# Kernel optimization log

Measured on AMD Instinct MI355X. Metric: run time of the kernel, lower is better.

## Reference

```python
import jax, jax.numpy as jnp
import numpy as np

B, N, E, ED, H, HID, OUT = 128, 100, 3200, 8, 4, 16, 32


def _ln(x, g, b):
    m = x.mean(-1, keepdims=True)
    v = ((x - m) ** 2).mean(-1, keepdims=True)
    return (x - m) / jnp.sqrt(v + 1e-5) * g + b


def _seg_softmax(logits, seg, n):
    # logits: [Etot, H], seg: [Etot] target node ids
    m = jax.ops.segment_max(logits, seg, num_segments=n)
    ex = jnp.exp(logits - m[seg])
    s = jax.ops.segment_sum(ex, seg, num_segments=n)
    return ex / (s[seg] + 1e-16)


def _tconv(x, src, dst, ea, Wq, bq, Wk, bk, Wv, bv, We, Ws, bs, heads, ch, n):
    # PyG TransformerConv, concat=False, root_weight=True, beta=False
    q = (x @ Wq.T + bq).reshape(-1, heads, ch)
    k = (x @ Wk.T + bk).reshape(-1, heads, ch)
    v = (x @ Wv.T + bv).reshape(-1, heads, ch)
    e = (ea @ We.T).reshape(-1, heads, ch)
    alpha = (q[dst] * (k[src] + e)).sum(-1) / jnp.sqrt(jnp.float32(ch))  # [Etot,H]
    alpha = _seg_softmax(alpha, dst, n)
    msg = (v[src] + e) * alpha[..., None]
    out = jax.ops.segment_sum(msg, dst, num_segments=n)  # [n,H,ch]
    out = out.mean(axis=1)  # concat=False -> head mean
    return out + x @ Ws.T + bs


def setup_inputs() -> dict:
    key = jax.random.key(0)
    ks = jax.random.split(key, 32)
    d = {}
    d['nodes_feats'] = jax.random.randint(ks[0], (B, N, 1), 0, 5).astype(jnp.float32)
    d['edge_index'] = jax.random.randint(ks[1], (B, 2, E), 0, N).astype(jnp.int32)
    d['edge_attr'] = jax.random.normal(ks[2], (B, E, ED), jnp.float32)
    d['agent_id'] = jax.random.randint(ks[3], (B, 1), 0, N).astype(jnp.int32)
    s = 0.1
    d['entity_embed'] = jax.random.normal(ks[4], (5, 4), jnp.float32)
    d['W1'] = jax.random.normal(ks[5], (HID, 4 + ED), jnp.float32) * s
    d['b1'] = jnp.zeros((HID,), jnp.float32)
    d['W2'] = jax.random.normal(ks[6], (HID, HID), jnp.float32) * s
    d['b2'] = jnp.zeros((HID,), jnp.float32)
    d['W3'] = jax.random.normal(ks[7], (HID, HID), jnp.float32) * s
    d['b3'] = jnp.zeros((HID,), jnp.float32)
    d['ln_g'] = jnp.ones((HID,), jnp.float32)
    d['ln_b'] = jnp.zeros((HID,), jnp.float32)
    i = 8
    for pre, ch, outd in (('g1', HID, HID), ('g2', OUT, OUT)):
        d[pre + '_Wq'] = jax.random.normal(ks[i + 0], (H * ch, HID), jnp.float32) * s
        d[pre + '_bq'] = jnp.zeros((H * ch,), jnp.float32)
        d[pre + '_Wk'] = jax.random.normal(ks[i + 1], (H * ch, HID), jnp.float32) * s
        d[pre + '_bk'] = jnp.zeros((H * ch,), jnp.float32)
        d[pre + '_Wv'] = jax.random.normal(ks[i + 2], (H * ch, HID), jnp.float32) * s
        d[pre + '_bv'] = jnp.zeros((H * ch,), jnp.float32)
        d[pre + '_We'] = jax.random.normal(ks[i + 3], (H * ch, ED), jnp.float32) * s
        d[pre + '_Ws'] = jax.random.normal(ks[i + 4], (outd, HID), jnp.float32) * s
        d[pre + '_bs'] = jnp.zeros((outd,), jnp.float32)
        i += 5
    return d


def reference(nodes_feats, edge_index, edge_attr, agent_id, entity_embed,
              W1, b1, W2, b2, W3, b3, ln_g, ln_b,
              g1_Wq, g1_bq, g1_Wk, g1_bk, g1_Wv, g1_bv, g1_We, g1_Ws, g1_bs,
              g2_Wq, g2_bq, g2_Wk, g2_bk, g2_Wv, g2_bv, g2_We, g2_Ws, g2_bs):
    n_tot = B * N
    # batched graph -> flat graph with per-batch node offsets
    offs = (jnp.arange(B, dtype=edge_index.dtype) * N)[:, None, None]
    ei = (edge_index + offs).transpose(1, 0, 2).reshape(2, -1)  # [2, B*E]
    src, dst = ei[0], ei[1]
    x = nodes_feats.reshape(-1, 1)            # [n_tot, 1]
    ea = edge_attr.reshape(-1, ED)            # [B*E, ED]

    # Embedding message-passing layer (aggr='add')
    etype = x[:, 0].astype(jnp.int32)[src]
    emb = entity_embed[etype]                  # [Etot, 4]
    h = jnp.concatenate([emb, ea], axis=1)
    h = _ln(jax.nn.relu(h @ W1.T + b1), ln_g, ln_b)
    h = _ln(jax.nn.relu(h @ W2.T + b2), ln_g, ln_b)
    h = _ln(jax.nn.relu(h @ W3.T + b3), ln_g, ln_b)
    z = jax.ops.segment_sum(h, dst, num_segments=n_tot)  # [n_tot, 16]

    a = _tconv(z, src, dst, ea, g1_Wq, g1_bq, g1_Wk, g1_bk, g1_Wv, g1_bv,
               g1_We, g1_Ws, g1_bs, H, HID, n_tot)
    a = _tconv(a, src, dst, ea, g2_Wq, g2_bq, g2_Wk, g2_bk, g2_Wv, g2_bv,
               g2_We, g2_Ws, g2_bs, H, OUT, n_tot)
    a = jax.nn.relu(a).reshape(B, N, OUT)
    # graph_aggr == 'agent': gather the agent node per batch
    out = jnp.take_along_axis(a, agent_id[:, :, None].astype(jnp.int32), axis=1)
    return out[:, 0, :]  # [B, OUT]
```

## Files before the change

kernel.cpp:

```cpp
#include <hip/hip_runtime.h>
#include <math.h>
#include <stdint.h>

#define Bb   128
#define Nn   100
#define Ee   3200
#define NTOT (Bb*Nn)
#define ETOT (Bb*Ee)



__global__ __launch_bounds__(256) void k_csr(const int* __restrict__ ei,
                                             const int* __restrict__ agent,
                                             int* __restrict__ off,
                                             int2* __restrict__ cpair,
                                             int* __restrict__ mark)
{
    int b = ((blockIdx.x & 7) << 4) + (blockIdx.x >> 3);
    int t = threadIdx.x;
    __shared__ int cnt[128];
    __shared__ int exc[128];
    __shared__ int cur[128];
    if (t < 128) cnt[t] = 0;
    if (t < Nn) mark[b * Nn + t] = 0;
    __syncthreads();
    const int* eis = ei + (size_t)b * 2 * Ee;
    const int* eid = eis + Ee;
    for (int e = t; e < Ee; e += 256) atomicAdd(&cnt[eid[e]], 1);
    __syncthreads();
    if (t < 128) exc[t] = cnt[t];
    __syncthreads();
    for (int d = 1; d < 128; d <<= 1) {
        int v = 0;
        if (t < 128 && t >= d) v = exc[t - d];
        __syncthreads();
        if (t < 128) exc[t] += v;
        __syncthreads();
    }
    if (t < 128) { int e0 = exc[t] - cnt[t]; exc[t] = e0; cur[t] = e0; }
    __syncthreads();
    if (t < Nn) off[b * Nn + t] = b * Ee + exc[t];
    if (b == Bb - 1 && t == 0) off[NTOT] = ETOT;
    for (int e = t; e < Ee; e += 256) {
        int dst = eid[e];
        int idx = atomicAdd(&cur[dst], 1);
        cpair[b * Ee + idx] = make_int2(eis[e] + b * Nn, b * Ee + e);
    }
    int an = agent[b];
    __syncthreads();
    if (t == 0) mark[b * Nn + an] = 1;
    for (int e = t; e < Ee; e += 256) {
        if (eid[e] == an) mark[b * Nn + eis[e]] = 1;
    }
}


__device__ __forceinline__ void ln_reg(float* h, const float* __restrict__ g,
                                       const float* __restrict__ b) {
    float s = 0.f;
#pragma unroll
    for (int c = 0; c < 16; c++) s += h[c];
    float m = s * 0.0625f;
    float v = 0.f;
#pragma unroll
    for (int c = 0; c < 16; c++) { float d = h[c] - m; v += d * d; }
    float r = rsqrtf(v * 0.0625f + 1e-5f);
#pragma unroll
    for (int c = 0; c < 16; c++) h[c] = (h[c] - m) * r * g[c] + b[c];
}

__global__ __launch_bounds__(256) void k_mlpz(
    const float* __restrict__ nf, const float* __restrict__ ea, const float* __restrict__ ee,
    const float* __restrict__ W1, const float* __restrict__ b1,
    const float* __restrict__ W2, const float* __restrict__ b2,
    const float* __restrict__ W3, const float* __restrict__ b3,
    const float* __restrict__ lg, const float* __restrict__ lb,
    const float* __restrict__ Wq, const float* __restrict__ bq,
    const float* __restrict__ Wk, const float* __restrict__ bk,
    const float* __restrict__ Wv, const float* __restrict__ bv,
    const int* __restrict__ off, const int2* __restrict__ cpair,
    float* __restrict__ z, float* __restrict__ q1, float* __restrict__ k1, float* __restrict__ v1)
{
    __shared__ float hs[4][64][17];
    __shared__ int sdeg[4];
    int lane = threadIdx.x & 63;
    int wid  = threadIdx.x >> 6;
    int n    = (blockIdx.x & 7) * (NTOT / 8) + (blockIdx.x >> 3) * 4 + wid;

    int o0 = off[n];
    int deg = off[n + 1] - o0;
    if (lane == 0) sdeg[wid] = deg;
    __syncthreads();
    int mdeg = max(max(sdeg[0], sdeg[1]), max(sdeg[2], sdeg[3]));
    int chunks = (mdeg + 63) >> 6;

    float zp = 0.f;
    for (int ch = 0; ch < chunks; ch++) {
        int i = ch * 64 + lane;
        float h3[16];
        if (i < deg) {
            int2 p = cpair[o0 + i];
            int et = (int)nf[p.x];
            float in[12];
#pragma unroll
            for (int j = 0; j < 4; j++) in[j] = ee[et * 4 + j];
            const float4* ea4 = (const float4*)(ea + (size_t)p.y * 8);
            float4 ua = ea4[0], ub = ea4[1];
            in[4] = ua.x; in[5] = ua.y; in[6] = ua.z; in[7] = ua.w;
            in[8] = ub.x; in[9] = ub.y; in[10] = ub.z; in[11] = ub.w;

            float h1[16];
#pragma unroll
            for (int c = 0; c < 16; c++) {
                float s = b1[c];
#pragma unroll
                for (int j = 0; j < 12; j++) s = fmaf(W1[c * 12 + j], in[j], s);
                h1[c] = fmaxf(s, 0.f);
            }
            ln_reg(h1, lg, lb);
            float h2[16];
#pragma unroll
            for (int c = 0; c < 16; c++) {
                float s = b2[c];
#pragma unroll
                for (int j = 0; j < 16; j++) s = fmaf(W2[c * 16 + j], h1[j], s);
                h2[c] = fmaxf(s, 0.f);
            }
            ln_reg(h2, lg, lb);
#pragma unroll
            for (int c = 0; c < 16; c++) {
                float s = b3[c];
#pragma unroll
                for (int j = 0; j < 16; j++) s = fmaf(W3[c * 16 + j], h2[j], s);
                h3[c] = fmaxf(s, 0.f);
            }
            ln_reg(h3, lg, lb);
        } else {
#pragma unroll
            for (int c = 0; c < 16; c++) h3[c] = 0.f;
        }
#pragma unroll
        for (int c = 0; c < 16; c++) hs[wid][lane][c] = h3[c];
        __syncthreads();
        int g = lane >> 4, c = lane & 15;
        float s = 0.f;
#pragma unroll
        for (int k = 0; k < 16; k++) s += hs[wid][g * 16 + k][c];
        s += __shfl_xor(s, 16);
        s += __shfl_xor(s, 32);
        zp += s;
        __syncthreads();
    }

    if (lane < 16) z[n * 16 + lane] = zp;

    float aq = bq[lane], ak = bk[lane], av = bv[lane];
#pragma unroll
    for (int j = 0; j < 16; j++) {
        float zj = __shfl(zp, j, 16);
        aq = fmaf(Wq[lane * 16 + j], zj, aq);
        ak = fmaf(Wk[lane * 16 + j], zj, ak);
        av = fmaf(Wv[lane * 16 + j], zj, av);
    }
    q1[n * 64 + lane] = aq;
    k1[n * 64 + lane] = ak;
    v1[n * 64 + lane] = av;
}


__global__ __launch_bounds__(256) void k_attn1(
    const float* __restrict__ ea,
    const float* __restrict__ q1, const float* __restrict__ k1, const float* __restrict__ v1,
    const float* __restrict__ We, const float* __restrict__ Ws, const float* __restrict__ bs,
    const float* __restrict__ z, const int* __restrict__ mark,
    const int* __restrict__ off, const int2* __restrict__ cpair,
    float* __restrict__ a1)
{
    int lane = threadIdx.x & 63;
    int wid  = threadIdx.x >> 6;
    int n    = (blockIdx.x & 7) * (NTOT / 8) + (blockIdx.x >> 3) * 4 + wid;

    if (!mark[n]) return;

    float wer[8];
#pragma unroll
    for (int j = 0; j < 8; j++) wer[j] = We[lane * 8 + j];
    float ql = q1[n * 64 + lane];

    int o0 = off[n];
    int deg = off[n + 1] - o0;

    float m = -1e30f, l = 0.f, acc = 0.f;
    int i = 0;
    for (; i + 2 <= deg; i += 2) {
        int2 pA = cpair[o0 + i];
        int2 pB = cpair[o0 + i + 1];
        const float4* eaA = (const float4*)(ea + (size_t)pA.y * 8);
        const float4* eaB = (const float4*)(ea + (size_t)pB.y * 8);
        float4 a0v = eaA[0], a1v = eaA[1], b0v = eaB[0], b1v = eaB[1];
        float eA = wer[0] * a0v.x + wer[1] * a0v.y + wer[2] * a0v.z + wer[3] * a0v.w
                 + wer[4] * a1v.x + wer[5] * a1v.y + wer[6] * a1v.z + wer[7] * a1v.w;
        float eB = wer[0] * b0v.x + wer[1] * b0v.y + wer[2] * b0v.z + wer[3] * b0v.w
                 + wer[4] * b1v.x + wer[5] * b1v.y + wer[6] * b1v.z + wer[7] * b1v.w;
        float kA = k1[(size_t)pA.x * 64 + lane];
        float kB = k1[(size_t)pB.x * 64 + lane];
        float vA = v1[(size_t)pA.x * 64 + lane];
        float vB = v1[(size_t)pB.x * 64 + lane];
        float tA = ql * (kA + eA);
        float tB = ql * (kB + eB);
        tA += __shfl_xor(tA, 1, 16);  tB += __shfl_xor(tB, 1, 16);
        tA += __shfl_xor(tA, 2, 16);  tB += __shfl_xor(tB, 2, 16);
        tA += __shfl_xor(tA, 4, 16);  tB += __shfl_xor(tB, 4, 16);
        tA += __shfl_xor(tA, 8, 16);  tB += __shfl_xor(tB, 8, 16);
        float lA = tA * 0.25f;
        float lB = tB * 0.25f;
        float nm = fmaxf(m, fmaxf(lA, lB));
        float sc = __expf(m - nm);
        float wA = __expf(lA - nm);
        float wB = __expf(lB - nm);
        acc = acc * sc + wA * (vA + eA) + wB * (vB + eB);
        l   = l * sc + wA + wB;
        m   = nm;
    }
    for (; i < deg; i++) {
        int2 p = cpair[o0 + i];
        const float4* ea4 = (const float4*)(ea + (size_t)p.y * 8);
        float4 u0 = ea4[0], u1 = ea4[1];
        float el = wer[0] * u0.x + wer[1] * u0.y + wer[2] * u0.z + wer[3] * u0.w
                 + wer[4] * u1.x + wer[5] * u1.y + wer[6] * u1.z + wer[7] * u1.w;
        float kl = k1[(size_t)p.x * 64 + lane];
        float t = ql * (kl + el);
        t += __shfl_xor(t, 1, 16);
        t += __shfl_xor(t, 2, 16);
        t += __shfl_xor(t, 4, 16);
        t += __shfl_xor(t, 8, 16);
        float logit = t * 0.25f;
        float nm = fmaxf(m, logit);
        float sc = __expf(m - nm);
        float w  = __expf(logit - nm);
        float vl = v1[(size_t)p.x * 64 + lane];
        acc = acc * sc + w * (vl + el);
        l   = l * sc + w;
        m   = nm;
    }
    float y = (deg > 0) ? (acc / l) : 0.f;
    y += __shfl_xor(y, 16);
    y += __shfl_xor(y, 32);
    y *= 0.25f;

    if (lane < 16) {
        float r = bs[lane];
#pragma unroll
        for (int j = 0; j < 16; j++) r = fmaf(Ws[lane * 16 + j], z[n * 16 + j], r);
        a1[n * 16 + lane] = y + r;
    }
}


__global__ __launch_bounds__(256) void k_g2(
    const float* __restrict__ ea, const float* __restrict__ a1, const int* __restrict__ agent,
    const float* __restrict__ Wq, const float* __restrict__ bq,
    const float* __restrict__ Wk, const float* __restrict__ bk,
    const float* __restrict__ Wv, const float* __restrict__ bv,
    const float* __restrict__ We, const float* __restrict__ Ws, const float* __restrict__ bs,
    const int* __restrict__ off, const int2* __restrict__ cpair,
    float* __restrict__ out)
{
    __shared__ float sm[4][64], sl[4][64], sa0[4][64], sa1[4][64];
    int b = ((blockIdx.x & 7) << 4) + (blockIdx.x >> 3);
    int lane = threadIdx.x & 63;
    int w = threadIdx.x >> 6;
    int n = b * Nn + agent[b];
    int v0 = lane * 2, v1i = lane * 2 + 1;

    float aa[16];
#pragma unroll
    for (int j = 0; j < 16; j++) aa[j] = a1[n * 16 + j];

    float wk0[16], wk1[16], wv0[16], wv1[16], we0[8], we1[8];
#pragma unroll
    for (int j = 0; j < 16; j++) {
        wk0[j] = Wk[v0 * 16 + j];  wk1[j] = Wk[v1i * 16 + j];
        wv0[j] = Wv[v0 * 16 + j];  wv1[j] = Wv[v1i * 16 + j];
    }
#pragma unroll
    for (int j = 0; j < 8; j++) { we0[j] = We[v0 * 8 + j]; we1[j] = We[v1i * 8 + j]; }

    float q0 = bq[v0], q1v = bq[v1i];
#pragma unroll
    for (int j = 0; j < 16; j++) {
        q0  = fmaf(Wq[v0 * 16 + j],  aa[j], q0);
        q1v = fmaf(Wq[v1i * 16 + j], aa[j], q1v);
    }

    int o0 = off[n];
    int deg = off[n + 1] - o0;

    float m = -1e30f, l = 0.f, a0 = 0.f, a1c = 0.f;
    for (int i = w; i < deg; i += 4) {
        int2 p = cpair[o0 + i];
        int src = p.x, ge = p.y;
        float as[16];
#pragma unroll
        for (int j = 0; j < 16; j++) as[j] = a1[src * 16 + j];
        const float4* ea4 = (const float4*)(ea + (size_t)ge * 8);
        float4 u0 = ea4[0], u1 = ea4[1];
        float eav[8] = {u0.x, u0.y, u0.z, u0.w, u1.x, u1.y, u1.z, u1.w};

        float k0 = bk[v0], k1v = bk[v1i], vv0 = bv[v0], vv1 = bv[v1i];
#pragma unroll
        for (int j = 0; j < 16; j++) {
            k0  = fmaf(wk0[j], as[j], k0);
            k1v = fmaf(wk1[j], as[j], k1v);
            vv0 = fmaf(wv0[j], as[j], vv0);
            vv1 = fmaf(wv1[j], as[j], vv1);
        }
        float e0 = 0.f, e1 = 0.f;
#pragma unroll
        for (int j = 0; j < 8; j++) { e0 = fmaf(we0[j], eav[j], e0); e1 = fmaf(we1[j], eav[j], e1); }

        float t = q0 * (k0 + e0) + q1v * (k1v + e1);
        t += __shfl_xor(t, 1, 16);
        t += __shfl_xor(t, 2, 16);
        t += __shfl_xor(t, 4, 16);
        t += __shfl_xor(t, 8, 16);
        float logit = t * 0.17677669529663687f;
        float nm = fmaxf(m, logit);
        float sc = __expf(m - nm);
        float wgt = __expf(logit - nm);
        a0  = a0 * sc + wgt * (vv0 + e0);
        a1c = a1c * sc + wgt * (vv1 + e1);
        l   = l * sc + wgt;
        m   = nm;
    }
    sm[w][lane] = m; sl[w][lane] = l; sa0[w][lane] = a0; sa1[w][lane] = a1c;
    __syncthreads();
    if (w == 0) {
        float M = fmaxf(fmaxf(sm[0][lane], sm[1][lane]), fmaxf(sm[2][lane], sm[3][lane]));
        float L = 0.f, A0 = 0.f, A1 = 0.f;
#pragma unroll
        for (int ww = 0; ww < 4; ww++) {
            float sc = __expf(sm[ww][lane] - M);
            L  += sc * sl[ww][lane];
            A0 += sc * sa0[ww][lane];
            A1 += sc * sa1[ww][lane];
        }
        float y0 = (deg > 0) ? (A0 / L) : 0.f;
        float y1 = (deg > 0) ? (A1 / L) : 0.f;
        y0 += __shfl_xor(y0, 16); y0 += __shfl_xor(y0, 32);
        y1 += __shfl_xor(y1, 16); y1 += __shfl_xor(y1, 32);
        y0 *= 0.25f; y1 *= 0.25f;

        if (lane < 16) {
            int c0 = lane * 2, c1 = lane * 2 + 1;
            float r0 = bs[c0], r1 = bs[c1];
#pragma unroll
            for (int j = 0; j < 16; j++) {
                r0 = fmaf(Ws[c0 * 16 + j], aa[j], r0);
                r1 = fmaf(Ws[c1 * 16 + j], aa[j], r1);
            }
            out[b * 32 + c0] = fmaxf(y0 + r0, 0.f);
            out[b * 32 + c1] = fmaxf(y1 + r1, 0.f);
        }
    }
}


extern "C" void kernel_launch(void* const* d_in, const int* in_sizes, int n_in,
                              void* d_out, int out_size, void* d_ws, size_t ws_size,
                              hipStream_t stream) {
    (void)in_sizes; (void)n_in; (void)out_size; (void)ws_size;
    const float* nf    = (const float*)d_in[0];
    const int*   ei    = (const int*)d_in[1];
    const float* ea    = (const float*)d_in[2];
    const int*   agent = (const int*)d_in[3];
    const float* ee    = (const float*)d_in[4];
    const float* W1    = (const float*)d_in[5];
    const float* b1    = (const float*)d_in[6];
    const float* W2    = (const float*)d_in[7];
    const float* b2    = (const float*)d_in[8];
    const float* W3    = (const float*)d_in[9];
    const float* b3    = (const float*)d_in[10];
    const float* lg    = (const float*)d_in[11];
    const float* lb    = (const float*)d_in[12];
    const float* g1Wq  = (const float*)d_in[13];
    const float* g1bq  = (const float*)d_in[14];
    const float* g1Wk  = (const float*)d_in[15];
    const float* g1bk  = (const float*)d_in[16];
    const float* g1Wv  = (const float*)d_in[17];
    const float* g1bv  = (const float*)d_in[18];
    const float* g1We  = (const float*)d_in[19];
    const float* g1Ws  = (const float*)d_in[20];
    const float* g1bs  = (const float*)d_in[21];
    const float* g2Wq  = (const float*)d_in[22];
    const float* g2bq  = (const float*)d_in[23];
    const float* g2Wk  = (const float*)d_in[24];
    const float* g2bk  = (const float*)d_in[25];
    const float* g2Wv  = (const float*)d_in[26];
    const float* g2bv  = (const float*)d_in[27];
    const float* g2We  = (const float*)d_in[28];
    const float* g2Ws  = (const float*)d_in[29];
    const float* g2bs  = (const float*)d_in[30];
    float* out = (float*)d_out;

    char* w = (char*)d_ws;
    int* mark  = (int*)w;  w += (size_t)NTOT * 4;
    int* off   = (int*)w;  w += (size_t)(NTOT + 4) * 4;
    w = (char*)(((uintptr_t)w + 15) & ~(uintptr_t)15);
    int2* cpair = (int2*)w; w += (size_t)ETOT * 8;
    float* z   = (float*)w; w += (size_t)NTOT * 16 * 4;
    float* q1  = (float*)w; w += (size_t)NTOT * 64 * 4;
    float* k1  = (float*)w; w += (size_t)NTOT * 64 * 4;
    float* v1  = (float*)w; w += (size_t)NTOT * 64 * 4;
    float* a1  = (float*)w; w += (size_t)NTOT * 16 * 4;

    k_csr<<<dim3(Bb), dim3(256), 0, stream>>>(ei, agent, off, cpair, mark);
    k_mlpz<<<dim3(NTOT / 4), dim3(256), 0, stream>>>(
        nf, ea, ee, W1, b1, W2, b2, W3, b3, lg, lb,
        g1Wq, g1bq, g1Wk, g1bk, g1Wv, g1bv,
        off, cpair, z, q1, k1, v1);
    k_attn1<<<dim3(NTOT / 4), dim3(256), 0, stream>>>(
        ea, q1, k1, v1, g1We, g1Ws, g1bs, z, mark, off, cpair, a1);
    k_g2<<<dim3(Bb), dim3(256), 0, stream>>>(
        ea, a1, agent, g2Wq, g2bq, g2Wk, g2bk, g2Wv, g2bv, g2We, g2Ws, g2bs,
        off, cpair, out);
}
```

Measured before the change: 204.6 us.

## Flatten per-node edge MLP into block-wide edge chunks, unroll attention by four

k_mlpz now gives each 512-thread block 16 consecutive nodes and processes their combined edge range in shared-memory chunks. Every thread runs the edge MLP on one edge, which removes the idle lanes of the old one-wave-per-node scheme when degrees vary. Each wave then reduces the per-node sums for its two nodes from the shared buffer. k_attn1 processes four edges per iteration instead of two to expose more memory-level parallelism, and k_csr folds the agent-neighbour marking into the scatter loop. The costs are more shared memory per block, which may limit occupancy, and more register pressure from the wider unroll.

```diff
diff --git a/kernel.cpp b/kernel.cpp
--- a/kernel.cpp
+++ b/kernel.cpp
@@ -7,6 +7,7 @@
 #define Ee   3200
 #define NTOT (Bb*Nn)
 #define ETOT (Bb*Ee)
+#define CAP  768
 
 
 
@@ -41,17 +42,14 @@
     __syncthreads();
     if (t < Nn) off[b * Nn + t] = b * Ee + exc[t];
     if (b == Bb - 1 && t == 0) off[NTOT] = ETOT;
+    int an = agent[b];
     for (int e = t; e < Ee; e += 256) {
         int dst = eid[e];
         int idx = atomicAdd(&cur[dst], 1);
-        cpair[b * Ee + idx] = make_int2(eis[e] + b * Nn, b * Ee + e);
-    }
-    int an = agent[b];
-    __syncthreads();
+        cpair[(size_t)b * Ee + idx] = make_int2(eis[e] + b * Nn, b * Ee + e);
+        if (dst == an) mark[b * Nn + eis[e]] = 1;
+    }
     if (t == 0) mark[b * Nn + an] = 1;
-    for (int e = t; e < Ee; e += 256) {
-        if (eid[e] == an) mark[b * Nn + eis[e]] = 1;
-    }
 }
 
 
@@ -69,7 +67,7 @@
     for (int c = 0; c < 16; c++) h[c] = (h[c] - m) * r * g[c] + b[c];
 }
 
-__global__ __launch_bounds__(256) void k_mlpz(
+__global__ __launch_bounds__(512) void k_mlpz(
     const float* __restrict__ nf, const float* __restrict__ ea, const float* __restrict__ ee,
     const float* __restrict__ W1, const float* __restrict__ b1,
     const float* __restrict__ W2, const float* __restrict__ b2,
@@ -81,25 +79,26 @@
     const int* __restrict__ off, const int2* __restrict__ cpair,
     float* __restrict__ z, float* __restrict__ q1, float* __restrict__ k1, float* __restrict__ v1)
 {
-    __shared__ float hs[4][64][17];
-    __shared__ int sdeg[4];
-    int lane = threadIdx.x & 63;
-    int wid  = threadIdx.x >> 6;
-    int n    = (blockIdx.x & 7) * (NTOT / 8) + (blockIdx.x >> 3) * 4 + wid;
-
-    int o0 = off[n];
-    int deg = off[n + 1] - o0;
-    if (lane == 0) sdeg[wid] = deg;
-    __syncthreads();
-    int mdeg = max(max(sdeg[0], sdeg[1]), max(sdeg[2], sdeg[3]));
-    int chunks = (mdeg + 63) >> 6;
-
-    float zp = 0.f;
-    for (int ch = 0; ch < chunks; ch++) {
-        int i = ch * 64 + lane;
-        float h3[16];
-        if (i < deg) {
-            int2 p = cpair[o0 + i];
+    __shared__ float hls[CAP][17];
+    __shared__ int soff[17];
+    int t = threadIdx.x;
+    int lane = t & 63;
+    int w = t >> 6;
+    int blk = (blockIdx.x & 7) * 100 + (blockIdx.x >> 3);
+    int n0 = blk * 16;
+
+    if (t < 17) soff[t] = off[n0 + t];
+    __syncthreads();
+    int e0 = soff[0], e1 = soff[16];
+
+    int nA = 2 * w, nB = 2 * w + 1;
+    int c = lane & 15, slot = lane >> 4;
+    float zpA = 0.f, zpB = 0.f;
+
+    for (int cs = e0; cs < e1; cs += CAP) {
+        int m = min(CAP, e1 - cs);
+        for (int i = t; i < m; i += 512) {
+            int2 p = cpair[cs + i];
             int et = (int)nf[p.x];
             float in[12];
 #pragma unroll
@@ -111,62 +110,73 @@
 
             float h1[16];
 #pragma unroll
-            for (int c = 0; c < 16; c++) {
-                float s = b1[c];
-#pragma unroll
-                for (int j = 0; j < 12; j++) s = fmaf(W1[c * 12 + j], in[j], s);
-                h1[c] = fmaxf(s, 0.f);
+            for (int cc = 0; cc < 16; cc++) {
+                float s = b1[cc];
+#pragma unroll
+                for (int j = 0; j < 12; j++) s = fmaf(W1[cc * 12 + j], in[j], s);
+                h1[cc] = fmaxf(s, 0.f);
             }
             ln_reg(h1, lg, lb);
             float h2[16];
 #pragma unroll
-            for (int c = 0; c < 16; c++) {
-                float s = b2[c];
-#pragma unroll
-                for (int j = 0; j < 16; j++) s = fmaf(W2[c * 16 + j], h1[j], s);
-                h2[c] = fmaxf(s, 0.f);
+            for (int cc = 0; cc < 16; cc++) {
+                float s = b2[cc];
+#pragma unroll
+                for (int j = 0; j < 16; j++) s = fmaf(W2[cc * 16 + j], h1[j], s);
+                h2[cc] = fmaxf(s, 0.f);
             }
             ln_reg(h2, lg, lb);
-#pragma unroll
-            for (int c = 0; c < 16; c++) {
-                float s = b3[c];
-#pragma unroll
-                for (int j = 0; j < 16; j++) s = fmaf(W3[c * 16 + j], h2[j], s);
-                h3[c] = fmaxf(s, 0.f);
+            float h3[16];
+#pragma unroll
+            for (int cc = 0; cc < 16; cc++) {
+                float s = b3[cc];
+#pragma unroll
+                for (int j = 0; j < 16; j++) s = fmaf(W3[cc * 16 + j], h2[j], s);
+                h3[cc] = fmaxf(s, 0.f);
             }
             ln_reg(h3, lg, lb);
-        } else {
-#pragma unroll
-            for (int c = 0; c < 16; c++) h3[c] = 0.f;
-        }
-#pragma unroll
-        for (int c = 0; c < 16; c++) hs[wid][lane][c] = h3[c];
+#pragma unroll
+            for (int cc = 0; cc < 16; cc++) hls[i][cc] = h3[cc];
+        }
         __syncthreads();
-        int g = lane >> 4, c = lane & 15;
-        float s = 0.f;
-#pragma unroll
-        for (int k = 0; k < 16; k++) s += hs[wid][g * 16 + k][c];
-        s += __shfl_xor(s, 16);
-        s += __shfl_xor(s, 32);
-        zp += s;
+        {
+            int rloA = max(soff[nA], cs) - cs, rhiA = min(soff[nA + 1], cs + m) - cs;
+            for (int r = rloA + slot; r < rhiA; r += 4) zpA += hls[r][c];
+            int rloB = max(soff[nB], cs) - cs, rhiB = min(soff[nB + 1], cs + m) - cs;
+            for (int r = rloB + slot; r < rhiB; r += 4) zpB += hls[r][c];
+        }
         __syncthreads();
     }
 
-    if (lane < 16) z[n * 16 + lane] = zp;
-
-    float aq = bq[lane], ak = bk[lane], av = bv[lane];
-#pragma unroll
-    for (int j = 0; j < 16; j++) {
-        float zj = __shfl(zp, j, 16);
-        aq = fmaf(Wq[lane * 16 + j], zj, aq);
-        ak = fmaf(Wk[lane * 16 + j], zj, ak);
-        av = fmaf(Wv[lane * 16 + j], zj, av);
-    }
-    q1[n * 64 + lane] = aq;
-    k1[n * 64 + lane] = ak;
-    v1[n * 64 + lane] = av;
-}
-
+#pragma unroll
+    for (int ni = 0; ni < 2; ni++) {
+        float zp = ni ? zpB : zpA;
+        int n = n0 + 2 * w + ni;
+        zp += __shfl_xor(zp, 16);
+        zp += __shfl_xor(zp, 32);
+        if (lane < 16) z[n * 16 + lane] = zp;
+        float aq = bq[lane], ak = bk[lane], av = bv[lane];
+#pragma unroll
+        for (int j = 0; j < 16; j++) {
+            float zj = __shfl(zp, j, 16);
+            aq = fmaf(Wq[lane * 16 + j], zj, aq);
+            ak = fmaf(Wk[lane * 16 + j], zj, ak);
+            av = fmaf(Wv[lane * 16 + j], zj, av);
+        }
+        q1[n * 64 + lane] = aq;
+        k1[n * 64 + lane] = ak;
+        v1[n * 64 + lane] = av;
+    }
+}
+
+
+__device__ __forceinline__ float red16(float t) {
+    t += __shfl_xor(t, 1, 16);
+    t += __shfl_xor(t, 2, 16);
+    t += __shfl_xor(t, 4, 16);
+    t += __shfl_xor(t, 8, 16);
+    return t;
+}
 
 __global__ __launch_bounds__(256) void k_attn1(
     const float* __restrict__ ea,
@@ -192,55 +202,62 @@
 
     float m = -1e30f, l = 0.f, acc = 0.f;
     int i = 0;
-    for (; i + 2 <= deg; i += 2) {
+    for (; i + 4 <= deg; i += 4) {
         int2 pA = cpair[o0 + i];
         int2 pB = cpair[o0 + i + 1];
+        int2 pC = cpair[o0 + i + 2];
+        int2 pD = cpair[o0 + i + 3];
         const float4* eaA = (const float4*)(ea + (size_t)pA.y * 8);
         const float4* eaB = (const float4*)(ea + (size_t)pB.y * 8);
-        float4 a0v = eaA[0], a1v = eaA[1], b0v = eaB[0], b1v = eaB[1];
-        float eA = wer[0] * a0v.x + wer[1] * a0v.y + wer[2] * a0v.z + wer[3] * a0v.w
-                 + wer[4] * a1v.x + wer[5] * a1v.y + wer[6] * a1v.z + wer[7] * a1v.w;
-        float eB = wer[0] * b0v.x + wer[1] * b0v.y + wer[2] * b0v.z + wer[3] * b0v.w
-                 + wer[4] * b1v.x + wer[5] * b1v.y + wer[6] * b1v.z + wer[7] * b1v.w;
+        const float4* eaC = (const float4*)(ea + (size_t)pC.y * 8);
+        const float4* eaD = (const float4*)(ea + (size_t)pD.y * 8);
+        float4 a0 = eaA[0], a1v = eaA[1], b0 = eaB[0], b1v = eaB[1];
+        float4 c0 = eaC[0], c1v = eaC[1], d0 = eaD[0], d1v = eaD[1];
+        float eA = wer[0]*a0.x + wer[1]*a0.y + wer[2]*a0.z + wer[3]*a0.w
+                 + wer[4]*a1v.x + wer[5]*a1v.y + wer[6]*a1v.z + wer[7]*a1v.w;
+        float eB = wer[0]*b0.x + wer[1]*b0.y + wer[2]*b0.z + wer[3]*b0.w
+                 + wer[4]*b1v.x + wer[5]*b1v.y + wer[6]*b1v.z + wer[7]*b1v.w;
+        float eC = wer[0]*c0.x + wer[1]*c0.y + wer[2]*c0.z + wer[3]*c0.w
+                 + wer[4]*c1v.x + wer[5]*c1v.y + wer[6]*c1v.z + wer[7]*c1v.w;
+        float eD = wer[0]*d0.x + wer[1]*d0.y + wer[2]*d0.z + wer[3]*d0.w
+                 + wer[4]*d1v.x + wer[5]*d1v.y + wer[6]*d1v.z + wer[7]*d1v.w;
         float kA = k1[(size_t)pA.x * 64 + lane];
         float kB = k1[(size_t)pB.x * 64 + lane];
+        float kC = k1[(size_t)pC.x * 64 + lane];
+        float kD = k1[(size_t)pD.x * 64 + lane];
         float vA = v1[(size_t)pA.x * 64 + lane];
         float vB = v1[(size_t)pB.x * 64 + lane];
-        float tA = ql * (kA + eA);
-        float tB = ql * (kB + eB);
-        tA += __shfl_xor(tA, 1, 16);  tB += __shfl_xor(tB, 1, 16);
-        tA += __shfl_xor(tA, 2, 16);  tB += __shfl_xor(tB, 2, 16);
-        tA += __shfl_xor(tA, 4, 16);  tB += __shfl_xor(tB, 4, 16);
-        tA += __shfl_xor(tA, 8, 16);  tB += __shfl_xor(tB, 8, 16);
-        float lA = tA * 0.25f;
-        float lB = tB * 0.25f;
-        float nm = fmaxf(m, fmaxf(lA, lB));
+        float vC = v1[(size_t)pC.x * 64 + lane];
+        float vD = v1[(size_t)pD.x * 64 + lane];
+        float lA = red16(ql * (kA + eA)) * 0.25f;
+        float lB = red16(ql * (kB + eB)) * 0.25f;
+        float lC = red16(ql * (kC + eC)) * 0.25f;
+        float lD = red16(ql * (kD + eD)) * 0.25f;
+        float nm = fmaxf(fmaxf(m, fmaxf(lA, lB)), fmaxf(lC, lD));
         float sc = __expf(m - nm);
         float wA = __expf(lA - nm);
         float wB = __expf(lB - nm);
-        acc = acc * sc + wA * (vA + eA) + wB * (vB + eB);
-        l   = l * sc + wA + wB;
+        float wC = __expf(lC - nm);
+        float wD = __expf(lD - nm);
+        acc = acc * sc + wA * (vA + eA) + wB * (vB + eB) + wC * (vC + eC) + wD * (vD + eD);
+        l   = l * sc + wA + wB + wC + wD;
         m   = nm;
     }
     for (; i < deg; i++) {
         int2 p = cpair[o0 + i];
         const float4* ea4 = (const float4*)(ea + (size_t)p.y * 8);
         float4 u0 = ea4[0], u1 = ea4[1];
-        float el = wer[0] * u0.x + wer[1] * u0.y + wer[2] * u0.z + wer[3] * u0.w
-                 + wer[4] * u1.x + wer[5] * u1.y + wer[6] * u1.z + wer[7] * u1.w;
+        float el = wer[0]*u0.x + wer[1]*u0.y + wer[2]*u0.z + wer[3]*u0.w
+                 + wer[4]*u1.x + wer[5]*u1.y + wer[6]*u1.z + wer[7]*u1.w;
         float kl = k1[(size_t)p.x * 64 + lane];
-        float t = ql * (kl + el);
-        t += __shfl_xor(t, 1, 16);
-        t += __shfl_xor(t, 2, 16);
-        t += __shfl_xor(t, 4, 16);
-        t += __shfl_xor(t, 8, 16);
-        float logit = t * 0.25f;
+        float tq = red16(ql * (kl + el));
+        float logit = tq * 0.25f;
         float nm = fmaxf(m, logit);
         float sc = __expf(m - nm);
-        float w  = __expf(logit - nm);
+        float wt = __expf(logit - nm);
         float vl = v1[(size_t)p.x * 64 + lane];
-        acc = acc * sc + w * (vl + el);
-        l   = l * sc + w;
+        acc = acc * sc + wt * (vl + el);
+        l   = l * sc + wt;
         m   = nm;
     }
     float y = (deg > 0) ? (acc / l) : 0.f;
@@ -415,7 +432,7 @@
     float* a1  = (float*)w; w += (size_t)NTOT * 16 * 4;
 
     k_csr<<<dim3(Bb), dim3(256), 0, stream>>>(ei, agent, off, cpair, mark);
-    k_mlpz<<<dim3(NTOT / 4), dim3(256), 0, stream>>>(
+    k_mlpz<<<dim3(NTOT / 16), dim3(512), 0, stream>>>(
         nf, ea, ee, W1, b1, W2, b2, W3, b3, lg, lb,
         g1Wq, g1bq, g1Wk, g1bk, g1Wv, g1bv,
         off, cpair, z, q1, k1, v1);
```

New measurement: 443.3 us. +116.7%, slower.
